# Kernel tuning notes

Hardware: AMD Instinct MI355X
Metric: run time of the kernel (lower is better)

## Reference

```python
import jax, jax.numpy as jnp
import numpy as np


def setup_inputs() -> dict:
    key = jax.random.key(0)
    k1, k2 = jax.random.split(key)
    query = jax.random.normal(k1, (16, 256, 32, 32), dtype=jnp.float32)
    search_map = jax.random.normal(k2, (16, 256, 64, 64), dtype=jnp.float32)
    return {"query": query, "search_map": search_map}


def reference(query, search_map):
    # query: [bs, c, h, w]; search_map: [bs, c, H, W]
    bs, c, h, w = query.shape
    # pad H and W by h//2, w//2 on each side (matches F.pad(left,right,top,bottom))
    padded = jnp.pad(search_map, ((0, 0), (0, 0), (h // 2, h // 2), (w // 2, w // 2)))

    def corr_one(map_, q_):
        # map_: [c, Hp, Wp], q_: [c, h, w]
        # per-sample cross-correlation: the query acts as a single-output conv kernel
        out = jax.lax.conv_general_dilated(
            map_[None],            # [1, c, Hp, Wp]
            q_[None],              # [1, c, h, w] -> OIHW
            window_strides=(1, 1),
            padding="VALID",
            dimension_numbers=("NCHW", "OIHW", "NCHW"),
        )
        return out[0]              # [1, Hout, Wout]

    # vmap over the batch: each sample uses its own query as the kernel
    return jax.vmap(corr_one)(padded, query)  # [bs, 1, Hout, Wout]
```

## Files before the change

### kernel.cpp

```cpp
#include <hip/hip_runtime.h>
#include <stdint.h>

typedef __bf16 bf16x8 __attribute__((ext_vector_type(8)));
typedef float  f32x4  __attribute__((ext_vector_type(4)));
typedef uint32_t u32x4 __attribute__((ext_vector_type(4)));

__device__ __forceinline__ uint16_t f2bf(float f) {
    uint32_t u = __builtin_bit_cast(uint32_t, f);
    u += 0x7FFFu + ((u >> 16) & 1u);
    return (uint16_t)(u >> 16);
}

__global__ __launch_bounds__(256) void qtrans_kernel(const float* __restrict__ Q,
                                                     uint16_t* __restrict__ Qt,
                                                     float* __restrict__ out) {
    __shared__ float T[8 * 1064];
    const int ch = blockIdx.x, b = blockIdx.y;
    const int tid = threadIdx.x;

    {
        int g = (b * 32 + ch) * 256 + tid;
        if (g < 67600) out[g] = 0.f;
    }

    const float* src = Q + ((size_t)(b * 256 + ch * 8)) * 1024;
    #pragma unroll
    for (int it = 0; it < 32; ++it) {
        int r = tid + it * 256;
        int c8 = r >> 10, rem = r & 1023;
        T[c8 * 1064 + (rem >> 5) * 33 + (rem & 31)] = src[(size_t)c8 * 1024 + rem];
    }
    __syncthreads();

    uint32_t* dst = (uint32_t*)Qt;
    #pragma unroll
    for (int it = 0; it < 16; ++it) {
        int o2 = tid + it * 256;
        int t  = (o2 & 3) * 2;
        int il = (o2 >> 2) & 15;
        int j  = (o2 >> 6) & 31;
        int ih = (o2 >> 11) & 1;
        float v0 = T[t * 1064 + (ih * 16 + il) * 33 + j];
        float v1 = T[(t + 1) * 1064 + (ih * 16 + il) * 33 + j];
        uint32_t pk = (uint32_t)f2bf(v0) | ((uint32_t)f2bf(v1) << 16);
        size_t oi = ((((size_t)(b * 2 + ih) * 32 + j) * 32 + ch) * 16 + il) * 4 + (t >> 1);
        dst[oi] = pk;
    }
}

__global__ __launch_bounds__(256, 4) void corr_kernel(const float* __restrict__ S,
                                                      const uint16_t* __restrict__ Qt,
                                                      float* __restrict__ out) {
    __shared__ __align__(16) char smem[40960];
    uint16_t* S_l = (uint16_t*)smem;
    float*    Pw  = (float*)smem;

    const int bid = blockIdx.x;
    const int b = bid & 15, d = bid >> 4;
    const int tid = threadIdx.x, wave = tid >> 6, lane = tid & 63;
    const int l15 = lane & 15, l4 = lane >> 4;

    {
        const u32x4 z = {};
        for (int zi = tid; zi < 512; zi += 256) {
            int ch = zi >> 4, r = zi & 15;
            *(u32x4*)&S_l[ch * 640 + r * 8] = z;
        }
    }
    {
        const int sx = tid & 63, w = tid >> 6;
        const float* sp = S + ((size_t)b * 256) * 4096 + (size_t)d * 64;
        #pragma unroll
        for (int k = 0; k < 8; ++k) {
            int ch = w * 8 + k;
            float v[8];
            #pragma unroll
            for (int cc = 0; cc < 8; ++cc)
                v[cc] = sp[(size_t)(ch * 8 + cc) * 4096 + sx];
            u32x4 pk;
            #pragma unroll
            for (int q = 0; q < 4; ++q)
                pk[q] = (uint32_t)f2bf(v[2 * q]) | ((uint32_t)f2bf(v[2 * q + 1]) << 16);
            *(u32x4*)&S_l[ch * 640 + (sx + 16) * 8] = pk;
        }
    }
    __syncthreads();

    f32x4 acc[5][2] = {};

    #pragma unroll
    for (int jj = 0; jj < 4; ++jj) {
        const int j0a = wave + jj * 4;
        const uint16_t* qa0 = Qt + (((size_t)b * 2 + 0) * 32 + j0a) * 4096 + l4 * 128 + l15 * 8;
        const uint16_t* qa1 = Qt + (((size_t)b * 2 + 1) * 32 + j0a) * 4096 + l4 * 128 + l15 * 8;
        const uint16_t* qb0 = qa0 + 16 * 4096;
        const uint16_t* qb1 = qa1 + 16 * 4096;

        int rowt[5];
        #pragma unroll
        for (int t = 0; t < 5; ++t) {
            int rr = j0a + t * 16 + l15;
            rowt[t] = (rr < 80) ? rr : 0;
        }

        #pragma unroll
        for (int s = 0; s < 8; ++s) {
            bf16x8 Ba0 = *(const bf16x8*)(qa0 + s * 512);
            bf16x8 Ba1 = *(const bf16x8*)(qa1 + s * 512);
            bf16x8 Bb0 = *(const bf16x8*)(qb0 + s * 512);
            bf16x8 Bb1 = *(const bf16x8*)(qb1 + s * 512);
            const int chb = (s * 4 + l4) * 640;
            bf16x8 A[5];
            #pragma unroll
            for (int t = 0; t < 5; ++t)
                A[t] = *(const bf16x8*)&S_l[chb + rowt[t] * 8];
            #pragma unroll
            for (int t = 0; t < 5; ++t) {
                acc[t][0] = __builtin_amdgcn_mfma_f32_16x16x32_bf16(A[t], Ba0, acc[t][0], 0, 0, 0);
                acc[t][1] = __builtin_amdgcn_mfma_f32_16x16x32_bf16(A[t], Ba1, acc[t][1], 0, 0, 0);
            }
            #pragma unroll
            for (int t = 1; t < 5; ++t) {
                acc[t - 1][0] = __builtin_amdgcn_mfma_f32_16x16x32_bf16(A[t], Bb0, acc[t - 1][0], 0, 0, 0);
                acc[t - 1][1] = __builtin_amdgcn_mfma_f32_16x16x32_bf16(A[t], Bb1, acc[t - 1][1], 0, 0, 0);
            }
        }
    }

    __syncthreads();
    {
        float* pw = Pw + wave * 2560;
        #pragma unroll
        for (int m = 0; m < 5; ++m)
            #pragma unroll
            for (int n = 0; n < 2; ++n)
                *(f32x4*)&pw[(n * 16 + l15) * 80 + m * 16 + l4 * 4] = acc[m][n];
    }
    __syncthreads();
    for (int e = tid; e < 65 * 32; e += 256) {
        int x = e % 65, i = e / 65;
        int y = d - i + 16;
        if ((unsigned)y < 65u) {
            float v = Pw[0 * 2560 + i * 80 + x] + Pw[1 * 2560 + i * 80 + x]
                    + Pw[2 * 2560 + i * 80 + x] + Pw[3 * 2560 + i * 80 + x];
            atomicAdd(out + ((size_t)b * 4225 + (size_t)y * 65 + x), v);
        }
    }
}

__global__ __launch_bounds__(256) void naive_kernel(const float* __restrict__ Q,
                                                    const float* __restrict__ S,
                                                    float* __restrict__ out) {
    int gid = blockIdx.x * 256 + threadIdx.x;
    if (gid >= 67600) return;
    int b = gid / 4225, r = gid % 4225, y = r / 65, x = r % 65;
    int jlo = 16 - x; if (jlo < 0) jlo = 0;
    int jhi = 80 - x; if (jhi > 32) jhi = 32;
    float acc = 0.f;
    for (int c = 0; c < 256; ++c) {
        const float* Sb = S + ((size_t)(b * 256 + c)) * 4096;
        const float* Qb = Q + ((size_t)(b * 256 + c)) * 1024;
        for (int i = 0; i < 32; ++i) {
            int dd = y + i - 16;
            if ((unsigned)dd >= 64u) continue;
            const float* Sr = Sb + dd * 64 + (x - 16);
            const float* Qr = Qb + i * 32;
            for (int j = jlo; j < jhi; ++j) acc += Sr[j] * Qr[j];
        }
    }
    out[gid] = acc;
}

extern "C" void kernel_launch(void* const* d_in, const int* in_sizes, int n_in,
                              void* d_out, int out_size, void* d_ws, size_t ws_size,
                              hipStream_t stream) {
    (void)in_sizes; (void)n_in; (void)out_size;
    const float* Q = (const float*)d_in[0];
    const float* S = (const float*)d_in[1];
    float* out = (float*)d_out;

    const size_t QT_BYTES = (size_t)16 * 2 * 32 * 32 * 16 * 8 * 2;

    if (ws_size < QT_BYTES) {
        naive_kernel<<<(67600 + 255) / 256, 256, 0, stream>>>(Q, S, out);
        return;
    }
    uint16_t* Qt = (uint16_t*)d_ws;

    qtrans_kernel<<<dim3(32, 16), 256, 0, stream>>>(Q, Qt, out);
    corr_kernel<<<1024, 256, 0, stream>>>(S, Qt, out);
}
```

Baseline: 134.7 us.

## Software-pipeline query fragment loads and stagger channel order per wave

```diff
diff --git a/kernel.cpp b/kernel.cpp
--- a/kernel.cpp
+++ b/kernel.cpp
@@ -84,47 +84,60 @@
             *(u32x4*)&S_l[ch * 640 + (sx + 16) * 8] = pk;
         }
     }
+
+    const uint16_t* Bb = Qt + (size_t)b * 262144 + l4 * 128 + l15 * 8;
+
+    bf16x8 C0, C1, C2, C3;
+    {
+        const int s0 = (2 * wave) & 7;
+        const uint16_t* p0 = Bb + wave * 4096 + s0 * 512;
+        C0 = *(const bf16x8*)(p0);
+        C1 = *(const bf16x8*)(p0 + 131072);
+        C2 = *(const bf16x8*)(p0 + 65536);
+        C3 = *(const bf16x8*)(p0 + 196608);
+    }
+
     __syncthreads();
 
     f32x4 acc[5][2] = {};
 
     #pragma unroll
-    for (int jj = 0; jj < 4; ++jj) {
+    for (int n = 0; n < 32; ++n) {
+        const int jj = n >> 3;
+        const int s  = ((n & 7) + 2 * wave) & 7;
         const int j0a = wave + jj * 4;
-        const uint16_t* qa0 = Qt + (((size_t)b * 2 + 0) * 32 + j0a) * 4096 + l4 * 128 + l15 * 8;
-        const uint16_t* qa1 = Qt + (((size_t)b * 2 + 1) * 32 + j0a) * 4096 + l4 * 128 + l15 * 8;
-        const uint16_t* qb0 = qa0 + 16 * 4096;
-        const uint16_t* qb1 = qa1 + 16 * 4096;
-
-        int rowt[5];
+
+        const int nn = (n < 31) ? (n + 1) : 31;
+        const int jn = nn >> 3;
+        const int sn = ((nn & 7) + 2 * wave) & 7;
+        const uint16_t* pn = Bb + (wave + jn * 4) * 4096 + sn * 512;
+        bf16x8 N0 = *(const bf16x8*)(pn);
+        bf16x8 N1 = *(const bf16x8*)(pn + 131072);
+        bf16x8 N2 = *(const bf16x8*)(pn + 65536);
+        bf16x8 N3 = *(const bf16x8*)(pn + 196608);
+        __builtin_amdgcn_sched_barrier(0);
+
+        const int chb = (s * 4 + l4) * 640;
+        bf16x8 A[5];
         #pragma unroll
         for (int t = 0; t < 5; ++t) {
             int rr = j0a + t * 16 + l15;
-            rowt[t] = (rr < 80) ? rr : 0;
-        }
-
-        #pragma unroll
-        for (int s = 0; s < 8; ++s) {
-            bf16x8 Ba0 = *(const bf16x8*)(qa0 + s * 512);
-            bf16x8 Ba1 = *(const bf16x8*)(qa1 + s * 512);
-            bf16x8 Bb0 = *(const bf16x8*)(qb0 + s * 512);
-            bf16x8 Bb1 = *(const bf16x8*)(qb1 + s * 512);
-            const int chb = (s * 4 + l4) * 640;
-            bf16x8 A[5];
-            #pragma unroll
-            for (int t = 0; t < 5; ++t)
-                A[t] = *(const bf16x8*)&S_l[chb + rowt[t] * 8];
-            #pragma unroll
-            for (int t = 0; t < 5; ++t) {
-                acc[t][0] = __builtin_amdgcn_mfma_f32_16x16x32_bf16(A[t], Ba0, acc[t][0], 0, 0, 0);
-                acc[t][1] = __builtin_amdgcn_mfma_f32_16x16x32_bf16(A[t], Ba1, acc[t][1], 0, 0, 0);
-            }
-            #pragma unroll
-            for (int t = 1; t < 5; ++t) {
-                acc[t - 1][0] = __builtin_amdgcn_mfma_f32_16x16x32_bf16(A[t], Bb0, acc[t - 1][0], 0, 0, 0);
-                acc[t - 1][1] = __builtin_amdgcn_mfma_f32_16x16x32_bf16(A[t], Bb1, acc[t - 1][1], 0, 0, 0);
-            }
-        }
+            rr = (rr < 80) ? rr : 0;
+            A[t] = *(const bf16x8*)&S_l[chb + rr * 8];
+        }
+
+        #pragma unroll
+        for (int t = 0; t < 5; ++t) {
+            acc[t][0] = __builtin_amdgcn_mfma_f32_16x16x32_bf16(A[t], C0, acc[t][0], 0, 0, 0);
+            acc[t][1] = __builtin_amdgcn_mfma_f32_16x16x32_bf16(A[t], C1, acc[t][1], 0, 0, 0);
+        }
+        #pragma unroll
+        for (int t = 1; t < 5; ++t) {
+            acc[t - 1][0] = __builtin_amdgcn_mfma_f32_16x16x32_bf16(A[t], C2, acc[t - 1][0], 0, 0, 0);
+            acc[t - 1][1] = __builtin_amdgcn_mfma_f32_16x16x32_bf16(A[t], C3, acc[t - 1][1], 0, 0, 0);
+        }
+
+        C0 = N0; C1 = N1; C2 = N2; C3 = N3;
     }
 
     __syncthreads();
```

After: 132.7 us. Within noise of the previous version (-1.4%).
